# Kernel tuning notes

Measured on AMD Instinct MI355X. Metric: run time of the kernel, lower is better.

Reference implementation:

```python
import jax, jax.numpy as jnp
import numpy as np

NUM_CATEGORIES = 64
INPUT_DIM = 256
HIDDEN_DIM = 256
N = 4096  # number of samples (each with its own category)
M = 16    # rows per sample


def setup_inputs() -> dict:
    key = jax.random.key(0)
    k_x, k_cat, k_W = jax.random.split(key, 3)
    x = jax.random.normal(k_x, (N, M, INPUT_DIM), dtype=jnp.float32)
    cat_ids = jax.random.randint(k_cat, (N,), 0, NUM_CATEGORIES, dtype=jnp.int64)
    W = 0.02 * jax.random.normal(k_W, (NUM_CATEGORIES, INPUT_DIM, HIDDEN_DIM), dtype=jnp.float32)
    b = jnp.zeros((NUM_CATEGORIES, HIDDEN_DIM), dtype=jnp.float32)
    return {"x": x, "cat_ids": cat_ids, "W": W, "b": b}


def reference(x, cat_ids, W, b):
    # Gather per-sample weights/biases, then batched matmul + bias add.
    selected_W = W[cat_ids]              # [N, input_dim, hidden_dim]
    selected_b = b[cat_ids]              # [N, hidden_dim]
    out = jnp.einsum('nmi,nih->nmh', x, selected_W) + selected_b[:, None, :]
    return out
```

## Files before the change

kernel.cpp:

```cpp
#include <hip/hip_runtime.h>
#include <hip/hip_bf16.h>
#include <stdint.h>

#define N_SAMPLES 4096
#define M_ROWS 16
#define K_DIM 256
#define H_DIM 256
#define N_CATS 64
#define SPB 4
#define MAX_PADDED (N_SAMPLES + N_CATS * (SPB - 1))
#define NGROUP (MAX_PADDED / SPB)
#define GPX (NGROUP / 8)
#define GEMM_GRID (NGROUP * 2)
#define AROW 264

typedef _Float16 half8 __attribute__((ext_vector_type(8)));
typedef _Float16 half4 __attribute__((ext_vector_type(4)));
typedef float floatx4 __attribute__((ext_vector_type(4)));

#define WT_BYTES ((size_t)N_CATS * K_DIM * H_DIM * 2)
#define GCAT_OFF WT_BYTES
#define ORD_OFF  (WT_BYTES + 4288)
#define WS_NEED  (ORD_OFF + (size_t)MAX_PADDED * 4)

__global__ __launch_bounds__(256)
void prep_combined(const float* __restrict__ W, _Float16* __restrict__ Wt,
                   const int* __restrict__ cat, int* __restrict__ ord,
                   int* __restrict__ gcat) {
  const int tid = threadIdx.x;
  if (blockIdx.x < 1024) {
    __shared__ _Float16 t[64][72];
    const int bid = blockIdx.x;
    const int c  = bid >> 4;
    const int kb = (bid >> 2) & 3;
    const int hb = bid & 3;
    const int r  = tid >> 2;
    const int cg = (tid & 3) * 16;
    const float* src = W + ((size_t)c << 16) + (size_t)(kb * 64 + r) * 256 + hb * 64 + cg;
#pragma unroll
    for (int j = 0; j < 16; j += 4) {
      float4 v = *(const float4*)(src + j);
      t[r][cg + j + 0] = (_Float16)v.x;
      t[r][cg + j + 1] = (_Float16)v.y;
      t[r][cg + j + 2] = (_Float16)v.z;
      t[r][cg + j + 3] = (_Float16)v.w;
    }
    __syncthreads();
    _Float16* dst = Wt + ((size_t)c << 16) + (size_t)(hb * 64 + r) * 256 + kb * 64 + cg;
    half8 o0, o1;
#pragma unroll
    for (int j = 0; j < 8; j++) o0[j] = t[cg + j][r];
#pragma unroll
    for (int j = 0; j < 8; j++) o1[j] = t[cg + 8 + j][r];
    *(half8*)(dst) = o0;
    *(half8*)(dst + 8) = o1;
  } else {
    __shared__ int hist[N_CATS];
    __shared__ int poffs[N_CATS];
    __shared__ int curs[N_CATS];
    if (tid < N_CATS) hist[tid] = 0;
    for (int i = tid; i < MAX_PADDED; i += 256) ord[i] = -1;
    for (int i = tid; i < NGROUP; i += 256) gcat[i] = 0;
    __syncthreads();
    for (int i = tid; i < N_SAMPLES; i += 256) atomicAdd(&hist[cat[i]], 1);
    __syncthreads();
    if (tid == 0) {
      int run = 0;
      for (int c = 0; c < N_CATS; c++) {
        poffs[c] = run;
        run += ((hist[c] + SPB - 1) / SPB) * SPB;
      }
    }
    if (tid < N_CATS) curs[tid] = 0;
    __syncthreads();
    if (tid < N_CATS) {
      const int c = tid;
      const int g0 = poffs[c] >> 2;
      const int ng = (hist[c] + SPB - 1) >> 2;
      for (int g = 0; g < ng; g++) gcat[g0 + g] = c;
    }
    for (int i = tid; i < N_SAMPLES; i += 256) {
      int c = cat[i];
      int p = poffs[c] + atomicAdd(&curs[c], 1);
      ord[p] = i;
    }
  }
}

__global__ __launch_bounds__(256, 4)
void gemm_kernel(const float* __restrict__ x, const float* __restrict__ bias,
                 const _Float16* __restrict__ Wt, const int* __restrict__ ord,
                 const int* __restrict__ gcat, float* __restrict__ out) {
  __shared__ __align__(16) _Float16 sA[64 * AROW];

  const int tid = threadIdx.x;
  const int B = blockIdx.x;
  const int xcd = B & 7;
  const int slot = B >> 3;
  const int h_half = slot & 1;
  const int group = xcd * GPX + (slot >> 1);
  const int h0 = h_half << 7;

  const int cat = gcat[group];
  const int4 sm = *(const int4*)(ord + group * 4);
  if (sm.x < 0) return;

  const int wid  = tid >> 6;
  const int lane = tid & 63;
  const int l15  = lane & 15;
  const int quad = lane >> 4;

  const _Float16* wbase = Wt + ((size_t)cat << 16);

  half8 bf[8][2];
#pragma unroll
  for (int kt = 0; kt < 4; kt++)
#pragma unroll
    for (int nt = 0; nt < 2; nt++) {
      const int col = h0 + wid * 32 + nt * 16 + l15;
      bf[kt][nt] = *(const half8*)(wbase + (size_t)col * K_DIM + kt * 32 + quad * 8);
    }
  __builtin_amdgcn_sched_barrier(0);

  const int smp = (wid == 0) ? sm.x : (wid == 1) ? sm.y : (wid == 2) ? sm.z : sm.w;
  const float* asrc = (smp >= 0) ? (x + ((size_t)smp << 12)) : nullptr;
  _Float16* adst = sA + (size_t)(wid * 16) * AROW;
  if (asrc) {
#pragma unroll
    for (int j = 0; j < 16; j++) {
      float4 v = *(const float4*)(asrc + j * 256 + lane * 4);
      half4 h;
      h[0] = (_Float16)v.x; h[1] = (_Float16)v.y;
      h[2] = (_Float16)v.z; h[3] = (_Float16)v.w;
      *(half4*)(adst + (size_t)j * AROW + lane * 4) = h;
    }
  } else {
    half4 h;
#pragma unroll
    for (int e = 0; e < 4; e++) h[e] = (_Float16)0.0f;
#pragma unroll
    for (int j = 0; j < 16; j++)
      *(half4*)(adst + (size_t)j * AROW + lane * 4) = h;
  }

  floatx4 acc[4][2];
#pragma unroll
  for (int i = 0; i < 4; i++)
#pragma unroll
    for (int j = 0; j < 2; j++)
#pragma unroll
      for (int e = 0; e < 4; e++) acc[i][j][e] = 0.0f;

  __syncthreads();

#pragma unroll
  for (int kt = 0; kt < 8; kt++) {
    if (kt < 4) {
#pragma unroll
      for (int nt = 0; nt < 2; nt++) {
        const int col = h0 + wid * 32 + nt * 16 + l15;
        bf[kt + 4][nt] = *(const half8*)(wbase + (size_t)col * K_DIM + (kt + 4) * 32 + quad * 8);
      }
    }
    half8 af[4];
#pragma unroll
    for (int mt = 0; mt < 4; mt++)
      af[mt] = *(const half8*)&sA[(size_t)(mt * 16 + l15) * AROW + kt * 32 + quad * 8];
#pragma unroll
    for (int mt = 0; mt < 4; mt++)
#pragma unroll
      for (int nt = 0; nt < 2; nt++)
        acc[mt][nt] = __builtin_amdgcn_mfma_f32_16x16x32_f16(af[mt], bf[kt][nt], acc[mt][nt], 0, 0, 0);
  }

  float bv[2];
#pragma unroll
  for (int nt = 0; nt < 2; nt++)
    bv[nt] = bias[cat * H_DIM + h0 + wid * 32 + nt * 16 + l15];
  const int srow[4] = {sm.x, sm.y, sm.z, sm.w};
#pragma unroll
  for (int mt = 0; mt < 4; mt++) {
    const int s = srow[mt];
    if (s < 0) continue;
    float* obase = out + ((size_t)s << 12);
#pragma unroll
    for (int nt = 0; nt < 2; nt++) {
      const int col = h0 + wid * 32 + nt * 16 + l15;
#pragma unroll
      for (int rr = 0; rr < 4; rr++) {
        const int row = quad * 4 + rr;
        obase[(size_t)row * H_DIM + col] = acc[mt][nt][rr] + bv[nt];
      }
    }
  }
}

__global__ __launch_bounds__(256)
void naive_kernel(const float* __restrict__ x, const int* __restrict__ cat,
                  const float* __restrict__ W, const float* __restrict__ bias,
                  float* __restrict__ out) {
  __shared__ float sx[16 * 256];
  const int n = blockIdx.x;
  const int tid = threadIdx.x;
  const int c = cat[n];
  const float* xs = x + (size_t)n * 16 * 256;
  for (int i = tid; i < 16 * 256; i += 256) sx[i] = xs[i];
  __syncthreads();
  const float* Wc = W + ((size_t)c << 16);
  float accv[16];
  float bv = bias[c * 256 + tid];
#pragma unroll
  for (int m = 0; m < 16; m++) accv[m] = bv;
  for (int k = 0; k < 256; k++) {
    float w = Wc[(size_t)k * 256 + tid];
#pragma unroll
    for (int m = 0; m < 16; m++) accv[m] += sx[m * 256 + k] * w;
  }
#pragma unroll
  for (int m = 0; m < 16; m++) out[((size_t)n * 16 + m) * 256 + tid] = accv[m];
}

extern "C" void kernel_launch(void* const* d_in, const int* in_sizes, int n_in,
                              void* d_out, int out_size, void* d_ws, size_t ws_size,
                              hipStream_t stream) {
  const float* x    = (const float*)d_in[0];
  const int*   cat  = (const int*)d_in[1];
  const float* W    = (const float*)d_in[2];
  const float* bias = (const float*)d_in[3];
  float* out = (float*)d_out;

  if (ws_size < WS_NEED) {
    naive_kernel<<<N_SAMPLES, 256, 0, stream>>>(x, cat, W, bias, out);
    return;
  }

  char* ws = (char*)d_ws;
  _Float16* Wt = (_Float16*)ws;
  int* gcat = (int*)(ws + GCAT_OFF);
  int* ord  = (int*)(ws + ORD_OFF);

  prep_combined<<<1025, 256, 0, stream>>>(W, Wt, cat, ord, gcat);
  gemm_kernel<<<GEMM_GRID, 256, 0, stream>>>(x, bias, Wt, ord, gcat, out);
}
```

Before: 161.2 us.

## Make GEMM persistent per category with double-buffered activation prefetch

```diff
diff --git a/kernel.cpp b/kernel.cpp
--- a/kernel.cpp
+++ b/kernel.cpp
@@ -9,24 +9,23 @@
 #define N_CATS 64
 #define SPB 4
 #define MAX_PADDED (N_SAMPLES + N_CATS * (SPB - 1))
-#define NGROUP (MAX_PADDED / SPB)
-#define GPX (NGROUP / 8)
-#define GEMM_GRID (NGROUP * 2)
 #define AROW 264
+#define REPS 8
+#define GEMM_BLOCKS (N_CATS * REPS)
 
 typedef _Float16 half8 __attribute__((ext_vector_type(8)));
 typedef _Float16 half4 __attribute__((ext_vector_type(4)));
 typedef float floatx4 __attribute__((ext_vector_type(4)));
 
 #define WT_BYTES ((size_t)N_CATS * K_DIM * H_DIM * 2)
-#define GCAT_OFF WT_BYTES
-#define ORD_OFF  (WT_BYTES + 4288)
-#define WS_NEED  (ORD_OFF + (size_t)MAX_PADDED * 4)
+#define ORD_OFF  WT_BYTES
+#define POFF_OFF (ORD_OFF + (size_t)MAX_PADDED * 4)
+#define WS_NEED  (POFF_OFF + 65 * 4)
 
 __global__ __launch_bounds__(256)
 void prep_combined(const float* __restrict__ W, _Float16* __restrict__ Wt,
                    const int* __restrict__ cat, int* __restrict__ ord,
-                   int* __restrict__ gcat) {
+                   int* __restrict__ gpoffs) {
   const int tid = threadIdx.x;
   if (blockIdx.x < 1024) {
     __shared__ _Float16 t[64][72];
@@ -56,11 +55,10 @@
     *(half8*)(dst + 8) = o1;
   } else {
     __shared__ int hist[N_CATS];
-    __shared__ int poffs[N_CATS];
+    __shared__ int poffs[N_CATS + 1];
     __shared__ int curs[N_CATS];
     if (tid < N_CATS) hist[tid] = 0;
     for (int i = tid; i < MAX_PADDED; i += 256) ord[i] = -1;
-    for (int i = tid; i < NGROUP; i += 256) gcat[i] = 0;
     __syncthreads();
     for (int i = tid; i < N_SAMPLES; i += 256) atomicAdd(&hist[cat[i]], 1);
     __syncthreads();
@@ -70,15 +68,11 @@
         poffs[c] = run;
         run += ((hist[c] + SPB - 1) / SPB) * SPB;
       }
+      poffs[N_CATS] = run;
     }
     if (tid < N_CATS) curs[tid] = 0;
     __syncthreads();
-    if (tid < N_CATS) {
-      const int c = tid;
-      const int g0 = poffs[c] >> 2;
-      const int ng = (hist[c] + SPB - 1) >> 2;
-      for (int g = 0; g < ng; g++) gcat[g0 + g] = c;
-    }
+    if (tid <= N_CATS) gpoffs[tid] = poffs[tid];
     for (int i = tid; i < N_SAMPLES; i += 256) {
       int c = cat[i];
       int p = poffs[c] + atomicAdd(&curs[c], 1);
@@ -87,23 +81,23 @@
   }
 }
 
-__global__ __launch_bounds__(256, 4)
-void gemm_kernel(const float* __restrict__ x, const float* __restrict__ bias,
-                 const _Float16* __restrict__ Wt, const int* __restrict__ ord,
-                 const int* __restrict__ gcat, float* __restrict__ out) {
-  __shared__ __align__(16) _Float16 sA[64 * AROW];
+__global__ __launch_bounds__(512, 2)
+void gemm_persist(const float* __restrict__ x, const float* __restrict__ bias,
+                  const _Float16* __restrict__ Wt, const int* __restrict__ ord,
+                  const int* __restrict__ gpoffs, float* __restrict__ out) {
+  __shared__ __align__(16) _Float16 sA[2][64 * AROW];
 
   const int tid = threadIdx.x;
-  const int B = blockIdx.x;
-  const int xcd = B & 7;
-  const int slot = B >> 3;
-  const int h_half = slot & 1;
-  const int group = xcd * GPX + (slot >> 1);
-  const int h0 = h_half << 7;
-
-  const int cat = gcat[group];
-  const int4 sm = *(const int4*)(ord + group * 4);
-  if (sm.x < 0) return;
+  const int b = blockIdx.x;
+  const int xcd = b & 7;
+  const int kk = b >> 3;
+  const int cat = xcd * 8 + (kk >> 3);
+  const int rep = kk & 7;
+
+  const int gbeg = gpoffs[cat] >> 2;
+  const int gend = gpoffs[cat + 1] >> 2;
+  int g = gbeg + rep;
+  if (g >= gend) return;
 
   const int wid  = tid >> 6;
   const int lane = tid & 63;
@@ -114,84 +108,110 @@
 
   half8 bf[8][2];
 #pragma unroll
-  for (int kt = 0; kt < 4; kt++)
+  for (int kt = 0; kt < 8; kt++)
 #pragma unroll
     for (int nt = 0; nt < 2; nt++) {
-      const int col = h0 + wid * 32 + nt * 16 + l15;
+      const int col = wid * 32 + nt * 16 + l15;
       bf[kt][nt] = *(const half8*)(wbase + (size_t)col * K_DIM + kt * 32 + quad * 8);
     }
-  __builtin_amdgcn_sched_barrier(0);
-
-  const int smp = (wid == 0) ? sm.x : (wid == 1) ? sm.y : (wid == 2) ? sm.z : sm.w;
-  const float* asrc = (smp >= 0) ? (x + ((size_t)smp << 12)) : nullptr;
-  _Float16* adst = sA + (size_t)(wid * 16) * AROW;
-  if (asrc) {
-#pragma unroll
-    for (int j = 0; j < 16; j++) {
-      float4 v = *(const float4*)(asrc + j * 256 + lane * 4);
-      half4 h;
-      h[0] = (_Float16)v.x; h[1] = (_Float16)v.y;
-      h[2] = (_Float16)v.z; h[3] = (_Float16)v.w;
-      *(half4*)(adst + (size_t)j * AROW + lane * 4) = h;
-    }
-  } else {
+  float bv[2];
+#pragma unroll
+  for (int nt = 0; nt < 2; nt++)
+    bv[nt] = bias[cat * H_DIM + wid * 32 + nt * 16 + l15];
+
+  int4 sm = *(const int4*)(ord + g * 4);
+#pragma unroll
+  for (int j = 0; j < 8; j++) {
+    const int f = j * 512 + tid;
+    const int row = f >> 6;
+    const int col4 = f & 63;
+    const int s = (j >> 1) == 0 ? sm.x : (j >> 1) == 1 ? sm.y : (j >> 1) == 2 ? sm.z : sm.w;
+    float4 v = (s >= 0)
+        ? *(const float4*)(x + ((size_t)s << 12) + (size_t)(row & 15) * 256 + col4 * 4)
+        : make_float4(0.f, 0.f, 0.f, 0.f);
     half4 h;
-#pragma unroll
-    for (int e = 0; e < 4; e++) h[e] = (_Float16)0.0f;
-#pragma unroll
-    for (int j = 0; j < 16; j++)
-      *(half4*)(adst + (size_t)j * AROW + lane * 4) = h;
-  }
-
-  floatx4 acc[4][2];
-#pragma unroll
-  for (int i = 0; i < 4; i++)
-#pragma unroll
-    for (int j = 0; j < 2; j++)
-#pragma unroll
-      for (int e = 0; e < 4; e++) acc[i][j][e] = 0.0f;
-
+    h[0] = (_Float16)v.x; h[1] = (_Float16)v.y;
+    h[2] = (_Float16)v.z; h[3] = (_Float16)v.w;
+    *(half4*)&sA[0][row * AROW + col4 * 4] = h;
+  }
   __syncthreads();
 
-#pragma unroll
-  for (int kt = 0; kt < 8; kt++) {
-    if (kt < 4) {
+  int p = 0;
+  while (true) {
+    const int gn = g + REPS;
+    const bool has_next = (gn < gend);
+
+    int4 smn = sm;
+    float4 av[8];
+    if (has_next) {
+      smn = *(const int4*)(ord + gn * 4);
+#pragma unroll
+      for (int j = 0; j < 8; j++) {
+        const int f = j * 512 + tid;
+        const int row = f >> 6;
+        const int col4 = f & 63;
+        const int s = (j >> 1) == 0 ? smn.x : (j >> 1) == 1 ? smn.y : (j >> 1) == 2 ? smn.z : smn.w;
+        av[j] = (s >= 0)
+            ? *(const float4*)(x + ((size_t)s << 12) + (size_t)(row & 15) * 256 + col4 * 4)
+            : make_float4(0.f, 0.f, 0.f, 0.f);
+      }
+    }
+
+    floatx4 acc[4][2];
+#pragma unroll
+    for (int i = 0; i < 4; i++)
+#pragma unroll
+      for (int j = 0; j < 2; j++)
+#pragma unroll
+        for (int e = 0; e < 4; e++) acc[i][j][e] = 0.0f;
+#pragma unroll
+    for (int kt = 0; kt < 8; kt++) {
+      half8 af[4];
+#pragma unroll
+      for (int mt = 0; mt < 4; mt++)
+        af[mt] = *(const half8*)&sA[p][(mt * 16 + l15) * AROW + kt * 32 + quad * 8];
+#pragma unroll
+      for (int mt = 0; mt < 4; mt++)
+#pragma unroll
+        for (int nt = 0; nt < 2; nt++)
+          acc[mt][nt] = __builtin_amdgcn_mfma_f32_16x16x32_f16(af[mt], bf[kt][nt], acc[mt][nt], 0, 0, 0);
+    }
+
+    if (has_next) {
+#pragma unroll
+      for (int j = 0; j < 8; j++) {
+        const int f = j * 512 + tid;
+        const int row = f >> 6;
+        const int col4 = f & 63;
+        half4 h;
+        h[0] = (_Float16)av[j].x; h[1] = (_Float16)av[j].y;
+        h[2] = (_Float16)av[j].z; h[3] = (_Float16)av[j].w;
+        *(half4*)&sA[p ^ 1][row * AROW + col4 * 4] = h;
+      }
+    }
+
+    const int srow[4] = {sm.x, sm.y, sm.z, sm.w};
+#pragma unroll
+    for (int mt = 0; mt < 4; mt++) {
+      const int s = srow[mt];
+      if (s < 0) continue;
+      float* obase = out + ((size_t)s << 12);
 #pragma unroll
       for (int nt = 0; nt < 2; nt++) {
-        const int col = h0 + wid * 32 + nt * 16 + l15;
-        bf[kt + 4][nt] = *(const half8*)(wbase + (size_t)col * K_DIM + (kt + 4) * 32 + quad * 8);
-      }
-    }
-    half8 af[4];
-#pragma unroll
-    for (int mt = 0; mt < 4; mt++)
-      af[mt] = *(const half8*)&sA[(size_t)(mt * 16 + l15) * AROW + kt * 32 + quad * 8];
-#pragma unroll
-    for (int mt = 0; mt < 4; mt++)
-#pragma unroll
-      for (int nt = 0; nt < 2; nt++)
-        acc[mt][nt] = __builtin_amdgcn_mfma_f32_16x16x32_f16(af[mt], bf[kt][nt], acc[mt][nt], 0, 0, 0);
-  }
-
-  float bv[2];
-#pragma unroll
-  for (int nt = 0; nt < 2; nt++)
-    bv[nt] = bias[cat * H_DIM + h0 + wid * 32 + nt * 16 + l15];
-  const int srow[4] = {sm.x, sm.y, sm.z, sm.w};
-#pragma unroll
-  for (int mt = 0; mt < 4; mt++) {
-    const int s = srow[mt];
-    if (s < 0) continue;
-    float* obase = out + ((size_t)s << 12);
-#pragma unroll
-    for (int nt = 0; nt < 2; nt++) {
-      const int col = h0 + wid * 32 + nt * 16 + l15;
-#pragma unroll
-      for (int rr = 0; rr < 4; rr++) {
-        const int row = quad * 4 + rr;
-        obase[(size_t)row * H_DIM + col] = acc[mt][nt][rr] + bv[nt];
-      }
-    }
+        const int col = wid * 32 + nt * 16 + l15;
+#pragma unroll
+        for (int rr = 0; rr < 4; rr++) {
+          const int row = quad * 4 + rr;
+          obase[(size_t)row * H_DIM + col] = acc[mt][nt][rr] + bv[nt];
+        }
+      }
+    }
+
+    if (!has_next) break;
+    sm = smn;
+    g = gn;
+    p ^= 1;
+    __syncthreads();
   }
 }
 
@@ -236,9 +256,9 @@
 
   char* ws = (char*)d_ws;
   _Float16* Wt = (_Float16*)ws;
-  int* gcat = (int*)(ws + GCAT_OFF);
-  int* ord  = (int*)(ws + ORD_OFF);
-
-  prep_combined<<<1025, 256, 0, stream>>>(W, Wt, cat, ord, gcat);
-  gemm_kernel<<<GEMM_GRID, 256, 0, stream>>>(x, bias, Wt, ord, gcat, out);
-}
+  int* ord    = (int*)(ws + ORD_OFF);
+  int* gpoffs = (int*)(ws + POFF_OFF);
+
+  prep_combined<<<1025, 256, 0, stream>>>(W, Wt, cat, ord, gpoffs);
+  gemm_persist<<<GEMM_BLOCKS, 512, 0, stream>>>(x, bias, Wt, ord, gpoffs, out);
+}
```

Result: slower. 173.7 us (+7.8%).
